# Kernel tuning notes

Measured on AMD Instinct MI355X. Metric: run time of the kernel, lower is better.

The kernel has to match this reference:

```python
import jax, jax.numpy as jnp
import numpy as np

B, N_WAY, N_SHOT, QUERY, NUM_SLOT, D = 64, 5, 5, 15, 8, 640
LAMBDA = 0.1
NEG_INF = jnp.float32(-1e30)


def cover_select(scores):
    # scores: [b, n_way, num_slot]. For each class in order, greedily pick the
    # highest-scoring slot not already taken (replicates torch sort+dedup loop).
    def per_batch(s):
        def step(taken, row):
            sel = jnp.argmax(jnp.where(taken, NEG_INF, row))
            return taken.at[sel].set(True), sel
        _, sel = jax.lax.scan(step, jnp.zeros(s.shape[-1], dtype=bool), s)
        return sel  # [n_way]
    return jax.vmap(per_batch)(scores)  # [b, n_way]


def euclid(gallery, query):
    # gallery [b, n, d], query [b, m, d] -> [b, m, n]
    return jnp.sum((query[:, :, None, :] - gallery[:, None, :, :]) ** 2, axis=-1)


def loss_acc(proto, q, labels_query):
    diff = euclid(proto, q)                                   # [b, n_way*query, n_way]
    logits = jax.nn.log_softmax(-diff, axis=2)
    logits = logits.reshape(B, QUERY, N_WAY, N_WAY)
    nll = -jnp.take_along_axis(logits, labels_query, axis=3).mean()
    y_hat = jnp.argmax(logits, axis=3)
    acc = (y_hat == labels_query[..., 0]).astype(jnp.float32).mean()
    return nll, acc


def setup_inputs() -> dict:
    key = jax.random.key(0)
    k0, k1, k2, k3 = jax.random.split(key, 4)
    n_total = B * N_WAY * (N_SHOT + QUERY)
    out_f = jax.random.normal(k0, (n_total, NUM_SLOT, D), dtype=jnp.float32)
    labels_support = jax.random.randint(k1, (B, N_SHOT, N_WAY, 1), 0, N_WAY, dtype=jnp.int32)
    labels_query = jax.random.randint(k2, (B, QUERY, N_WAY, 1), 0, N_WAY, dtype=jnp.int32)
    att_loss = jax.random.uniform(k3, (1,), dtype=jnp.float32)
    return {"out_f": out_f, "labels_support": labels_support,
            "labels_query": labels_query, "att_loss": att_loss}


def reference(out_f, labels_support, labels_query, att_loss):
    # mode == 'train' path of SimilarityLoss.forward
    b, d = B, out_f.shape[-1]
    ns = b * N_WAY * N_SHOT
    # class prototypes over shots: [b*n_way, num_slot, d]
    sup = out_f[:ns].reshape(b * N_WAY, N_SHOT, NUM_SLOT, d).mean(1)
    qry = out_f[ns:].reshape(b, N_WAY, QUERY, NUM_SLOT, d)

    max_s = cover_select(sup.mean(-1).reshape(b, N_WAY, NUM_SLOT))  # [b, n_way]

    sup_b = sup.reshape(b, N_WAY, NUM_SLOT, d)
    # proto[j, c] = sup_b[j, c, max_s[j, c]]
    proto = jax.vmap(jax.vmap(lambda s, i: s[i]))(sup_b, max_s)     # [b, n_way, d]

    # get_selected path: each class's queries pick that class's selected slot
    out_query = jax.vmap(jax.vmap(lambda q, i: q[:, i, :]))(qry, max_s)  # [b, n_way, query, d]
    out_query = out_query.reshape(b, N_WAY * QUERY, d)

    # get_22 path (faithful to the original non-reset record_temp accumulation):
    # for image s, pick among rows {q22[j, s', max_s[j, i]] : s' <= s, i < n_way}
    # the row with the largest mean over d.
    imgs = N_WAY * QUERY
    q22 = qry.reshape(b, imgs, NUM_SLOT, d)
    cand = jax.vmap(lambda q, i: q[:, i, :])(q22, max_s)            # [b, imgs, n_way, d]
    L = imgs * N_WAY
    m = cand.mean(-1).reshape(b, L)                                 # flat order (s, i)
    prefix = jnp.arange(L)[None, :] < ((jnp.arange(imgs) + 1) * N_WAY)[:, None]  # [imgs, L]
    k = jnp.argmax(jnp.where(prefix[None], m[:, None, :], NEG_INF), axis=-1)     # [b, imgs]
    out_query_t = jnp.take_along_axis(cand.reshape(b, L, d), k[:, :, None], axis=1)  # [b, imgs, d]

    nll, acc = loss_acc(proto, out_query, labels_query)
    loss = nll + jnp.float32(LAMBDA) * att_loss[0]
    loss_t, acc_t = loss_acc(proto, out_query_t, labels_query)
    return (loss, loss_t, acc, acc_t)
```

## Files before the change

### kernel.cpp

```cpp
#include <hip/hip_runtime.h>

#define BB 64
#define N_WAY 5
#define N_SHOT 5
#define QUERY 15
#define NUM_SLOT 8
#define DD 640
#define IMGS (N_WAY * QUERY)
#define NS (BB * N_WAY * N_SHOT)
#define QROWS (BB * IMGS)
#define ROWSZ (NUM_SLOT * DD)
#define F4_PER_SLOT 160
#define NELEM (BB * IMGS)
#define NGROUP (BB * N_WAY)
#define PIECES 10
#define NBLK (BB * PIECES)

__global__ __launch_bounds__(256) void k_pass1(const float* __restrict__ out_f,
                                               float* __restrict__ rowmean_q,
                                               float* __restrict__ proto_all,
                                               float* __restrict__ pn2_all,
                                               float* __restrict__ supm_g) {
    int b = blockIdx.x;
    int t = threadIdx.x;
    int slot = t >> 5;
    int l = t & 31;
    if (b < NGROUP) {
        const int g = b;
        float4 acc[5];
        #pragma unroll
        for (int k = 0; k < 5; ++k) acc[k] = make_float4(0.f, 0.f, 0.f, 0.f);
        #pragma unroll
        for (int sh = 0; sh < N_SHOT; ++sh) {
            const float4* p = (const float4*)(out_f +
                ((size_t)((g * N_SHOT + sh) * NUM_SLOT + slot)) * DD);
            #pragma unroll
            for (int k = 0; k < 5; ++k) {
                float4 v = p[l + k * 32];
                acc[k].x += v.x; acc[k].y += v.y; acc[k].z += v.z; acc[k].w += v.w;
            }
        }
        float4* pp = (float4*)(proto_all + ((size_t)(g * NUM_SLOT + slot)) * DD);
        float ssq = 0.f, sm = 0.f;
        #pragma unroll
        for (int k = 0; k < 5; ++k) {
            acc[k].x *= 0.2f; acc[k].y *= 0.2f; acc[k].z *= 0.2f; acc[k].w *= 0.2f;
            pp[l + k * 32] = acc[k];
            ssq += acc[k].x * acc[k].x + acc[k].y * acc[k].y
                 + acc[k].z * acc[k].z + acc[k].w * acc[k].w;
            sm  += (acc[k].x + acc[k].y) + (acc[k].z + acc[k].w);
        }
        #pragma unroll
        for (int off = 16; off; off >>= 1) {
            ssq += __shfl_down(ssq, off, 32);
            sm  += __shfl_down(sm,  off, 32);
        }
        if (l == 0) {
            pn2_all[g * NUM_SLOT + slot] = ssq;
            supm_g[g * NUM_SLOT + slot]  = sm * (1.f / DD);
        }
    } else {
        int rq = b - NGROUP;
        const float4* p = (const float4*)(out_f + (size_t)(NS + rq) * ROWSZ)
                          + slot * F4_PER_SLOT;
        float s = 0.f;
        #pragma unroll
        for (int k = 0; k < 5; ++k) {
            float4 v = p[l + k * 32];
            s += (v.x + v.y) + (v.z + v.w);
        }
        #pragma unroll
        for (int off = 16; off; off >>= 1) s += __shfl_down(s, off, 32);
        if (l == 0) rowmean_q[rq * NUM_SLOT + slot] = s * (1.f / DD);
    }
}

__global__ __launch_bounds__(512) void k_mid(const float* __restrict__ out_f,
                                             const float* __restrict__ rowmean_q,
                                             const float* __restrict__ proto_all,
                                             const float* __restrict__ pn2_all,
                                             const float* __restrict__ supm_g,
                                             const int* __restrict__ labels_query,
                                             float4* __restrict__ part) {
    int b = blockIdx.x;
    int j = b / PIECES, piece = b - j * PIECES;
    int t = threadIdx.x;
    int wave = t >> 6, lane = t & 63;
    int m = piece * 8 + wave;

    __shared__ float qbt[NUM_SLOT][80];
    __shared__ float supmS[N_WAY * NUM_SLOT];
    __shared__ int   msS[N_WAY];
    __shared__ float p2S[N_WAY];
    __shared__ __align__(16) float2 protoS[N_WAY * 5][64];
    __shared__ float4 redS[8];

    const float* qbase = rowmean_q + (size_t)j * IMGS * NUM_SLOT;
    if (t < 150) {
        float4 v = ((const float4*)qbase)[t];
        int s = t >> 1, sl0 = (t & 1) * 4;
        qbt[sl0 + 0][s] = v.x; qbt[sl0 + 1][s] = v.y;
        qbt[sl0 + 2][s] = v.z; qbt[sl0 + 3][s] = v.w;
    }
    if (t >= 160 && t < 160 + N_WAY * NUM_SLOT)
        supmS[t - 160] = supm_g[j * (N_WAY * NUM_SLOT) + (t - 160)];
    __syncthreads();

    if (t == 0) {
        unsigned taken = 0u;
        #pragma unroll
        for (int c = 0; c < N_WAY; ++c) {
            float best = -3.0e38f; int bi = 0;
            #pragma unroll
            for (int s = 0; s < NUM_SLOT; ++s) {
                float v = supmS[c * NUM_SLOT + s];
                if (!((taken >> s) & 1u) && v > best) { best = v; bi = s; }
            }
            taken |= (1u << bi);
            msS[c] = bi;
        }
    }
    __syncthreads();

    int ms[N_WAY];
    #pragma unroll
    for (int n = 0; n < N_WAY; ++n) ms[n] = msS[n];
    if (t < N_WAY) p2S[t] = pn2_all[(j * N_WAY + t) * NUM_SLOT + ms[t]];

    float2 q1v[5];
    if (m < IMGS) {
        const float2* q1p = (const float2*)(out_f +
            (size_t)(NS + j * IMGS + m) * ROWSZ + ms[m / QUERY] * DD) + lane * 5;
        #pragma unroll
        for (int k = 0; k < 5; ++k) q1v[k] = q1p[k];
    }

    for (int idx = t; idx < N_WAY * 320; idx += 512) {
        int n = idx / 320, r = idx - n * 320;
        int lane_d = r / 5, k = r - lane_d * 5;
        const float2* gp = (const float2*)(proto_all +
            ((size_t)((j * N_WAY + n) * NUM_SLOT + ms[n])) * DD);
        protoS[n * 5 + k][lane_d] = gp[r];
    }

    float2 q2v[5];
    if (m < IMGS) {
        float bv = -3.0e38f; int bi = 0x7fffffff;
        #pragma unroll
        for (int rep = 0; rep < 2; ++rep) {
            int s = lane + rep * 64;
            if (s <= m) {
                #pragma unroll
                for (int c = 0; c < N_WAY; ++c) {
                    float x = qbt[ms[c]][s];
                    int flat = s * N_WAY + c;
                    if (x > bv || (x == bv && flat < bi)) { bv = x; bi = flat; }
                }
            }
        }
        #pragma unroll
        for (int off = 32; off; off >>= 1) {
            float ov = __shfl_down(bv, off, 64);
            int   oi = __shfl_down(bi, off, 64);
            if (ov > bv || (ov == bv && oi < bi)) { bv = ov; bi = oi; }
        }
        bi = __shfl(bi, 0, 64);
        int s2 = bi / N_WAY, c2 = bi - s2 * N_WAY;
        const float2* q2p = (const float2*)(out_f +
            (size_t)(NS + j * IMGS + s2) * ROWSZ + ms[c2] * DD) + lane * 5;
        #pragma unroll
        for (int k = 0; k < 5; ++k) q2v[k] = q2p[k];
    }
    __syncthreads();

    float4 lv = make_float4(0.f, 0.f, 0.f, 0.f);
    if (m < IMGS) {
        float s1[N_WAY] = {0, 0, 0, 0, 0};
        float s2a[N_WAY] = {0, 0, 0, 0, 0};
        #pragma unroll
        for (int n = 0; n < N_WAY; ++n) {
            #pragma unroll
            for (int k = 0; k < 5; ++k) {
                float2 p = protoS[n * 5 + k][lane];
                s1[n]  += q1v[k].x * p.x + q1v[k].y * p.y;
                s2a[n] += q2v[k].x * p.x + q2v[k].y * p.y;
            }
        }
        #pragma unroll
        for (int n = 0; n < N_WAY; ++n) {
            #pragma unroll
            for (int off = 32; off; off >>= 1) {
                s1[n]  += __shfl_down(s1[n],  off, 64);
                s2a[n] += __shfl_down(s2a[n], off, 64);
            }
        }
        if (lane == 0) {
            int label = labels_query[j * IMGS + m];
            {
                float li[N_WAY]; float mx = -3.0e38f;
                #pragma unroll
                for (int n = 0; n < N_WAY; ++n) { li[n] = 2.f * s1[n] - p2S[n]; mx = fmaxf(mx, li[n]); }
                float se = 0.f;
                #pragma unroll
                for (int n = 0; n < N_WAY; ++n) se += expf(li[n] - mx);
                float lse = mx + logf(se);
                int bn = 0; float bvv = li[0];
                #pragma unroll
                for (int n = 1; n < N_WAY; ++n) if (li[n] > bvv) { bvv = li[n]; bn = n; }
                lv.x = -(li[label] - lse);
                lv.z = (bn == label) ? 1.f : 0.f;
            }
            {
                float li[N_WAY]; float mx = -3.0e38f;
                #pragma unroll
                for (int n = 0; n < N_WAY; ++n) { li[n] = 2.f * s2a[n] - p2S[n]; mx = fmaxf(mx, li[n]); }
                float se = 0.f;
                #pragma unroll
                for (int n = 0; n < N_WAY; ++n) se += expf(li[n] - mx);
                float lse = mx + logf(se);
                int bn = 0; float bvv = li[0];
                #pragma unroll
                for (int n = 1; n < N_WAY; ++n) if (li[n] > bvv) { bvv = li[n]; bn = n; }
                lv.y = -(li[label] - lse);
                lv.w = (bn == label) ? 1.f : 0.f;
            }
        }
    }
    if (lane == 0) redS[wave] = lv;
    __syncthreads();
    if (t == 0) {
        float4 s = redS[0];
        #pragma unroll
        for (int w = 1; w < 8; ++w) {
            s.x += redS[w].x; s.y += redS[w].y; s.z += redS[w].z; s.w += redS[w].w;
        }
        part[b] = s;
    }
}

__global__ __launch_bounds__(256) void k_final(const float4* __restrict__ part,
                                               const float* __restrict__ att_loss,
                                               float* __restrict__ out) {
    __shared__ float4 red[256];
    int t = threadIdx.x;
    float4 s = make_float4(0.f, 0.f, 0.f, 0.f);
    for (int i = t; i < NBLK; i += 256) {
        float4 v = part[i];
        s.x += v.x; s.y += v.y; s.z += v.z; s.w += v.w;
    }
    red[t] = s;
    __syncthreads();
    for (int w = 128; w; w >>= 1) {
        if (t < w) {
            red[t].x += red[t + w].x; red[t].y += red[t + w].y;
            red[t].z += red[t + w].z; red[t].w += red[t + w].w;
        }
        __syncthreads();
    }
    if (t == 0) {
        out[0] = red[0].x / (float)NELEM + 0.1f * att_loss[0];
        out[1] = red[0].y / (float)NELEM;
        out[2] = red[0].z / (float)NELEM;
        out[3] = red[0].w / (float)NELEM;
    }
}

extern "C" void kernel_launch(void* const* d_in, const int* in_sizes, int n_in,
                              void* d_out, int out_size, void* d_ws, size_t ws_size,
                              hipStream_t stream) {
    const float* out_f        = (const float*)d_in[0];
    const int*   labels_query = (const int*)d_in[2];
    const float* att_loss     = (const float*)d_in[3];
    float* out = (float*)d_out;

    float*  rowmean_q = (float*)d_ws;
    float*  proto_all = rowmean_q + QROWS * NUM_SLOT;
    float*  pn2_all   = proto_all + NGROUP * NUM_SLOT * DD;
    float*  supm_g    = pn2_all + NGROUP * NUM_SLOT;
    float4* part      = (float4*)(supm_g + NGROUP * NUM_SLOT);

    k_pass1<<<NGROUP + QROWS, 256, 0, stream>>>(out_f, rowmean_q, proto_all,
                                                pn2_all, supm_g);
    k_mid<<<NBLK, 512, 0, stream>>>(out_f, rowmean_q, proto_all, pn2_all,
                                    supm_g, labels_query, part);
    k_final<<<1, 256, 0, stream>>>(part, att_loss, out);
}
```

Before: 42.47 us.

## Split slot selection and prefix argmax into separate kernel with wave-scan

Moves the greedy slot selection and the per-image prefix argmax out of k_mid into a small per-batch kernel k_sel. That kernel computes every prefix argmax once with an inclusive wave scan instead of a full reduction per image wave. k_mid then reads the precomputed indices and loads prototypes straight into registers instead of staging them through shared memory, and it runs smaller 256-thread blocks over more pieces. The aim is to remove redundant selection work and block-wide syncs in k_mid, at the cost of an extra kernel launch and repeated prototype loads from global/L2 memory.

```diff
diff --git a/kernel.cpp b/kernel.cpp
--- a/kernel.cpp
+++ b/kernel.cpp
@@ -13,7 +13,7 @@
 #define F4_PER_SLOT 160
 #define NELEM (BB * IMGS)
 #define NGROUP (BB * N_WAY)
-#define PIECES 10
+#define PIECES 19
 #define NBLK (BB * PIECES)
 
 __global__ __launch_bounds__(256) void k_pass1(const float* __restrict__ out_f,
@@ -75,115 +75,143 @@
     }
 }
 
-__global__ __launch_bounds__(512) void k_mid(const float* __restrict__ out_f,
-                                             const float* __restrict__ rowmean_q,
+__global__ __launch_bounds__(64) void k_sel(const float* __restrict__ rowmean_q,
+                                            const float* __restrict__ supm_g,
+                                            const float* __restrict__ pn2_all,
+                                            int* __restrict__ msel,
+                                            float* __restrict__ p2c,
+                                            int* __restrict__ k_idx) {
+    int j = blockIdx.x;
+    int t = threadIdx.x;
+    __shared__ float qbt[NUM_SLOT][80];
+    __shared__ float supmS[N_WAY * NUM_SLOT];
+    __shared__ int msS[N_WAY];
+
+    const float* qbase = rowmean_q + (size_t)j * IMGS * NUM_SLOT;
+    for (int i = t; i < 150; i += 64) {
+        float4 v = ((const float4*)qbase)[i];
+        int s = i >> 1, sl0 = (i & 1) * 4;
+        qbt[sl0 + 0][s] = v.x; qbt[sl0 + 1][s] = v.y;
+        qbt[sl0 + 2][s] = v.z; qbt[sl0 + 3][s] = v.w;
+    }
+    if (t < N_WAY * NUM_SLOT) supmS[t] = supm_g[j * (N_WAY * NUM_SLOT) + t];
+    __syncthreads();
+
+    if (t == 0) {
+        unsigned taken = 0u;
+        int packed = 0;
+        #pragma unroll
+        for (int c = 0; c < N_WAY; ++c) {
+            float best = -3.0e38f; int bi = 0;
+            #pragma unroll
+            for (int s = 0; s < NUM_SLOT; ++s) {
+                float v = supmS[c * NUM_SLOT + s];
+                if (!((taken >> s) & 1u) && v > best) { best = v; bi = s; }
+            }
+            taken |= (1u << bi);
+            msS[c] = bi;
+            packed |= bi << (3 * c);
+        }
+        msel[j] = packed;
+    }
+    __syncthreads();
+    int ms0 = msS[0], ms1 = msS[1], ms2 = msS[2], ms3 = msS[3], ms4 = msS[4];
+    if (t < N_WAY) p2c[j * N_WAY + t] = pn2_all[(j * N_WAY + t) * NUM_SLOT + msS[t]];
+
+    float bv; int bi;
+    {
+        bv = qbt[ms0][t]; bi = t * N_WAY;
+        float v;
+        v = qbt[ms1][t]; if (v > bv) { bv = v; bi = t * N_WAY + 1; }
+        v = qbt[ms2][t]; if (v > bv) { bv = v; bi = t * N_WAY + 2; }
+        v = qbt[ms3][t]; if (v > bv) { bv = v; bi = t * N_WAY + 3; }
+        v = qbt[ms4][t]; if (v > bv) { bv = v; bi = t * N_WAY + 4; }
+    }
+    #pragma unroll
+    for (int off = 1; off < 64; off <<= 1) {
+        float ov = __shfl_up(bv, off, 64);
+        int   oi = __shfl_up(bi, off, 64);
+        if (t >= off && !(bv > ov)) { bv = ov; bi = oi; }
+    }
+    k_idx[j * IMGS + t] = bi;
+    float tv = __shfl(bv, 63, 64);
+    int   ti = __shfl(bi, 63, 64);
+    float bv2 = -3.0e38f; int bi2 = 0;
+    if (t < IMGS - 64) {
+        int s = 64 + t;
+        bv2 = qbt[ms0][s]; bi2 = s * N_WAY;
+        float v;
+        v = qbt[ms1][s]; if (v > bv2) { bv2 = v; bi2 = s * N_WAY + 1; }
+        v = qbt[ms2][s]; if (v > bv2) { bv2 = v; bi2 = s * N_WAY + 2; }
+        v = qbt[ms3][s]; if (v > bv2) { bv2 = v; bi2 = s * N_WAY + 3; }
+        v = qbt[ms4][s]; if (v > bv2) { bv2 = v; bi2 = s * N_WAY + 4; }
+    }
+    #pragma unroll
+    for (int off = 1; off < 16; off <<= 1) {
+        float ov = __shfl_up(bv2, off, 64);
+        int   oi = __shfl_up(bi2, off, 64);
+        if (t >= off && t < IMGS - 64 && !(bv2 > ov)) { bv2 = ov; bi2 = oi; }
+    }
+    if (t < IMGS - 64) {
+        if (!(bv2 > tv)) { bv2 = tv; bi2 = ti; }
+        k_idx[j * IMGS + 64 + t] = bi2;
+    }
+}
+
+__global__ __launch_bounds__(256) void k_mid(const float* __restrict__ out_f,
                                              const float* __restrict__ proto_all,
-                                             const float* __restrict__ pn2_all,
-                                             const float* __restrict__ supm_g,
+                                             const int* __restrict__ msel,
+                                             const float* __restrict__ p2c,
+                                             const int* __restrict__ k_idx,
                                              const int* __restrict__ labels_query,
                                              float4* __restrict__ part) {
     int b = blockIdx.x;
     int j = b / PIECES, piece = b - j * PIECES;
     int t = threadIdx.x;
     int wave = t >> 6, lane = t & 63;
-    int m = piece * 8 + wave;
-
-    __shared__ float qbt[NUM_SLOT][80];
-    __shared__ float supmS[N_WAY * NUM_SLOT];
-    __shared__ int   msS[N_WAY];
-    __shared__ float p2S[N_WAY];
-    __shared__ __align__(16) float2 protoS[N_WAY * 5][64];
-    __shared__ float4 redS[8];
-
-    const float* qbase = rowmean_q + (size_t)j * IMGS * NUM_SLOT;
-    if (t < 150) {
-        float4 v = ((const float4*)qbase)[t];
-        int s = t >> 1, sl0 = (t & 1) * 4;
-        qbt[sl0 + 0][s] = v.x; qbt[sl0 + 1][s] = v.y;
-        qbt[sl0 + 2][s] = v.z; qbt[sl0 + 3][s] = v.w;
-    }
-    if (t >= 160 && t < 160 + N_WAY * NUM_SLOT)
-        supmS[t - 160] = supm_g[j * (N_WAY * NUM_SLOT) + (t - 160)];
-    __syncthreads();
-
-    if (t == 0) {
-        unsigned taken = 0u;
-        #pragma unroll
-        for (int c = 0; c < N_WAY; ++c) {
-            float best = -3.0e38f; int bi = 0;
-            #pragma unroll
-            for (int s = 0; s < NUM_SLOT; ++s) {
-                float v = supmS[c * NUM_SLOT + s];
-                if (!((taken >> s) & 1u) && v > best) { best = v; bi = s; }
-            }
-            taken |= (1u << bi);
-            msS[c] = bi;
-        }
-    }
-    __syncthreads();
-
+    int m = piece * 4 + wave;
+
+    __shared__ float4 redS[4];
+
+    int packed = msel[j];
     int ms[N_WAY];
     #pragma unroll
-    for (int n = 0; n < N_WAY; ++n) ms[n] = msS[n];
-    if (t < N_WAY) p2S[t] = pn2_all[(j * N_WAY + t) * NUM_SLOT + ms[t]];
-
-    float2 q1v[5];
+    for (int n = 0; n < N_WAY; ++n) ms[n] = (packed >> (3 * n)) & 7;
+
+    float4 lv = make_float4(0.f, 0.f, 0.f, 0.f);
     if (m < IMGS) {
+        int kk = k_idx[j * IMGS + m];
+        int s2 = kk / N_WAY, c2 = kk - s2 * N_WAY;
+
         const float2* q1p = (const float2*)(out_f +
             (size_t)(NS + j * IMGS + m) * ROWSZ + ms[m / QUERY] * DD) + lane * 5;
-        #pragma unroll
-        for (int k = 0; k < 5; ++k) q1v[k] = q1p[k];
-    }
-
-    for (int idx = t; idx < N_WAY * 320; idx += 512) {
-        int n = idx / 320, r = idx - n * 320;
-        int lane_d = r / 5, k = r - lane_d * 5;
-        const float2* gp = (const float2*)(proto_all +
-            ((size_t)((j * N_WAY + n) * NUM_SLOT + ms[n])) * DD);
-        protoS[n * 5 + k][lane_d] = gp[r];
-    }
-
-    float2 q2v[5];
-    if (m < IMGS) {
-        float bv = -3.0e38f; int bi = 0x7fffffff;
-        #pragma unroll
-        for (int rep = 0; rep < 2; ++rep) {
-            int s = lane + rep * 64;
-            if (s <= m) {
-                #pragma unroll
-                for (int c = 0; c < N_WAY; ++c) {
-                    float x = qbt[ms[c]][s];
-                    int flat = s * N_WAY + c;
-                    if (x > bv || (x == bv && flat < bi)) { bv = x; bi = flat; }
-                }
-            }
-        }
-        #pragma unroll
-        for (int off = 32; off; off >>= 1) {
-            float ov = __shfl_down(bv, off, 64);
-            int   oi = __shfl_down(bi, off, 64);
-            if (ov > bv || (ov == bv && oi < bi)) { bv = ov; bi = oi; }
-        }
-        bi = __shfl(bi, 0, 64);
-        int s2 = bi / N_WAY, c2 = bi - s2 * N_WAY;
         const float2* q2p = (const float2*)(out_f +
             (size_t)(NS + j * IMGS + s2) * ROWSZ + ms[c2] * DD) + lane * 5;
+        float2 q1v[5], q2v[5];
+        #pragma unroll
+        for (int k = 0; k < 5; ++k) q1v[k] = q1p[k];
         #pragma unroll
         for (int k = 0; k < 5; ++k) q2v[k] = q2p[k];
-    }
-    __syncthreads();
-
-    float4 lv = make_float4(0.f, 0.f, 0.f, 0.f);
-    if (m < IMGS) {
+
+        float2 pv[N_WAY][5];
+        float p2r[N_WAY];
+        #pragma unroll
+        for (int n = 0; n < N_WAY; ++n) {
+            const float2* pp = (const float2*)(proto_all +
+                ((size_t)((j * N_WAY + n) * NUM_SLOT + ms[n])) * DD) + lane * 5;
+            #pragma unroll
+            for (int k = 0; k < 5; ++k) pv[n][k] = pp[k];
+            p2r[n] = p2c[j * N_WAY + n];
+        }
+
         float s1[N_WAY] = {0, 0, 0, 0, 0};
         float s2a[N_WAY] = {0, 0, 0, 0, 0};
         #pragma unroll
         for (int n = 0; n < N_WAY; ++n) {
             #pragma unroll
             for (int k = 0; k < 5; ++k) {
-                float2 p = protoS[n * 5 + k][lane];
-                s1[n]  += q1v[k].x * p.x + q1v[k].y * p.y;
-                s2a[n] += q2v[k].x * p.x + q2v[k].y * p.y;
+                s1[n]  += q1v[k].x * pv[n][k].x + q1v[k].y * pv[n][k].y;
+                s2a[n] += q2v[k].x * pv[n][k].x + q2v[k].y * pv[n][k].y;
             }
         }
         #pragma unroll
@@ -199,7 +227,7 @@
             {
                 float li[N_WAY]; float mx = -3.0e38f;
                 #pragma unroll
-                for (int n = 0; n < N_WAY; ++n) { li[n] = 2.f * s1[n] - p2S[n]; mx = fmaxf(mx, li[n]); }
+                for (int n = 0; n < N_WAY; ++n) { li[n] = 2.f * s1[n] - p2r[n]; mx = fmaxf(mx, li[n]); }
                 float se = 0.f;
                 #pragma unroll
                 for (int n = 0; n < N_WAY; ++n) se += expf(li[n] - mx);
@@ -213,7 +241,7 @@
             {
                 float li[N_WAY]; float mx = -3.0e38f;
                 #pragma unroll
-                for (int n = 0; n < N_WAY; ++n) { li[n] = 2.f * s2a[n] - p2S[n]; mx = fmaxf(mx, li[n]); }
+                for (int n = 0; n < N_WAY; ++n) { li[n] = 2.f * s2a[n] - p2r[n]; mx = fmaxf(mx, li[n]); }
                 float se = 0.f;
                 #pragma unroll
                 for (int n = 0; n < N_WAY; ++n) se += expf(li[n] - mx);
@@ -229,12 +257,11 @@
     if (lane == 0) redS[wave] = lv;
     __syncthreads();
     if (t == 0) {
-        float4 s = redS[0];
-        #pragma unroll
-        for (int w = 1; w < 8; ++w) {
-            s.x += redS[w].x; s.y += redS[w].y; s.z += redS[w].z; s.w += redS[w].w;
-        }
-        part[b] = s;
+        float4 s0 = redS[0], s1 = redS[1], s2 = redS[2], s3 = redS[3];
+        part[b] = make_float4(s0.x + s1.x + s2.x + s3.x,
+                              s0.y + s1.y + s2.y + s3.y,
+                              s0.z + s1.z + s2.z + s3.z,
+                              s0.w + s1.w + s2.w + s3.w);
     }
 }
 
@@ -277,11 +304,15 @@
     float*  proto_all = rowmean_q + QROWS * NUM_SLOT;
     float*  pn2_all   = proto_all + NGROUP * NUM_SLOT * DD;
     float*  supm_g    = pn2_all + NGROUP * NUM_SLOT;
-    float4* part      = (float4*)(supm_g + NGROUP * NUM_SLOT);
+    float*  p2c       = supm_g + NGROUP * NUM_SLOT;
+    float4* part      = (float4*)(p2c + NGROUP);
+    int*    msel      = (int*)(part + NBLK);
+    int*    k_idx     = msel + BB;
 
     k_pass1<<<NGROUP + QROWS, 256, 0, stream>>>(out_f, rowmean_q, proto_all,
                                                 pn2_all, supm_g);
-    k_mid<<<NBLK, 512, 0, stream>>>(out_f, rowmean_q, proto_all, pn2_all,
-                                    supm_g, labels_query, part);
+    k_sel<<<BB, 64, 0, stream>>>(rowmean_q, supm_g, pn2_all, msel, p2c, k_idx);
+    k_mid<<<NBLK, 256, 0, stream>>>(out_f, proto_all, msel, p2c, k_idx,
+                                    labels_query, part);
     k_final<<<1, 256, 0, stream>>>(part, att_loss, out);
 }
```

After: 42.21 us. Within noise of the previous version (-0.6%).
